# Kernel optimization log

Hardware: AMD Instinct MI355X
Metric: run time of the kernel (lower is better)

## Reference

```python
import jax, jax.numpy as jnp
import numpy as np

B, T_AUX, UP = 4, 75, 110
N_AUX, N_Q, HID, SKIP = 54, 256, 192, 256
K, AUX_K = 6, 3
DIL_FACTS = [0, 1, 2] * 3  # dilation_depth=3, dilation_repeat=3
T = T_AUX * UP - 1  # 8249


def conv1d(x, w, b, dil=1, pad=(0, 0)):
    # x: (B,C,T), w: (O,I,K) torch Conv1d layout
    if pad != (0, 0):
        x = jnp.pad(x, ((0, 0), (0, 0), pad))
    y = jax.lax.conv_general_dilated(x, w, (1,), 'VALID', rhs_dilation=(dil,),
                                     dimension_numbers=('NCH', 'OIH', 'NCH'))
    return y + b[None, :, None]


def setup_inputs() -> dict:
    key = jax.random.key(0)
    ks = jax.random.split(key, 24)
    s = 0.05
    inp = {
        'audio': jax.random.normal(ks[0], (B, N_Q, T), jnp.float32),
        'aux': jax.random.normal(ks[1], (B, N_AUX, T_AUX), jnp.float32),
        'scale_in_w': jax.random.normal(ks[2], (N_AUX, N_AUX, 1), jnp.float32) * s,
        'scale_in_b': jax.random.normal(ks[3], (N_AUX,), jnp.float32) * s,
        'aux0_w': jax.random.normal(ks[4], (N_AUX * 3, N_AUX, AUX_K), jnp.float32) * s,
        'aux0_b': jax.random.normal(ks[5], (N_AUX * 3,), jnp.float32) * s,
        'aux1_w': jax.random.normal(ks[6], (N_AUX * 9, N_AUX * 3, AUX_K), jnp.float32) * s,
        'aux1_b': jax.random.normal(ks[7], (N_AUX * 9,), jnp.float32) * s,
        'up_w': jax.random.normal(ks[8], (UP,), jnp.float32) * s,
        'up_b': jax.random.normal(ks[9], (), jnp.float32) * s,
        'causal_w': jax.random.normal(ks[10], (HID, N_Q, K), jnp.float32) * s,
        'causal_b': jax.random.normal(ks[11], (HID,), jnp.float32) * s,
        'inx_w': jax.random.normal(ks[12], (9, 2 * HID, N_AUX * 9, 1), jnp.float32) * s,
        'inx_b': jax.random.normal(ks[13], (9, 2 * HID), jnp.float32) * s,
        'dilh_w': jax.random.normal(ks[14], (9, 2 * HID, HID, K), jnp.float32) * s,
        'dilh_b': jax.random.normal(ks[15], (9, 2 * HID), jnp.float32) * s,
        'skip_w': jax.random.normal(ks[16], (9, SKIP, HID, 1), jnp.float32) * s,
        'skip_b': jax.random.normal(ks[17], (9, SKIP), jnp.float32) * s,
        'out1_w': jax.random.normal(ks[18], (N_Q, SKIP, 1), jnp.float32) * s,
        'out1_b': jax.random.normal(ks[19], (N_Q,), jnp.float32) * s,
        'out2_w': jax.random.normal(ks[20], (N_Q, N_Q, 1), jnp.float32) * s,
        'out2_b': jax.random.normal(ks[21], (N_Q,), jnp.float32) * s,
    }
    return inp


def reference(audio, aux, scale_in_w, scale_in_b, aux0_w, aux0_b, aux1_w, aux1_b,
              up_w, up_b, causal_w, causal_b, inx_w, inx_b, dilh_w, dilh_b,
              skip_w, skip_b, out1_w, out1_b, out2_w, out2_b):
    # conditioning path: scale_in -> two-sided dilated convs -> deconv upsample
    a = conv1d(aux, scale_in_w, scale_in_b)
    a = conv1d(a, aux0_w, aux0_b, dil=1, pad=(1, 1))      # k=3, dil=1, same length
    a = conv1d(a, aux1_w, aux1_b, dil=3, pad=(3, 3))      # k=3, dil=3, same length
    b_, c_, t_ = a.shape
    x = (a[:, :, :, None] * up_w).reshape(b_, c_, t_ * UP) + up_b  # ConvTranspose2d(1,1,(1,UP))
    x = x[:, :, 1:]  # (B, 486, T)
    # audio path: causal conv (left pad k-1) + softsign
    h = jax.nn.soft_sign(conv1d(audio, causal_w, causal_b, dil=1, pad=(K - 1, 0)))
    sum_out = None
    for l, d in enumerate(DIL_FACTS):
        dil = K ** d
        lpad = dil * (K - 1)  # k**(d+1) - k**d
        xh = conv1d(x, inx_w[l], inx_b[l]) * conv1d(h, dilh_w[l], dilh_b[l], dil=dil, pad=(lpad, 0))
        z = jax.nn.sigmoid(xh[:, :HID])
        h = (1.0 - z) * jnp.tanh(xh[:, HID:]) + z * h
        skip = conv1d(h, skip_w[l], skip_b[l])
        sum_out = skip if sum_out is None else sum_out + skip
    out = conv1d(jax.nn.relu(sum_out), out1_w, out1_b)
    out = conv1d(jax.nn.relu(out), out2_w, out2_b)
    return out.transpose(0, 2, 1)  # (B, T, n_quantize)
```

## Files before the change

kernel.cpp:

```cpp
#include <hip/hip_runtime.h>

#define TLEN 8249
#define TPAD 8320
#define NTILES 130
#define NB 4
#define NAUX 54
#define NQ 256
#define HID 192
#define NSKIP 256
#define KW 6
#define UPF 110
#define TAUX 75
#define PADR 180
#define HROWS (PADR + TPAD)

typedef __attribute__((ext_vector_type(8))) short bf16x8v;
typedef __attribute__((ext_vector_type(4))) float f32x4;

__device__ __forceinline__ unsigned short f2bf(float f) {
  unsigned int u = __float_as_uint(f);
  u += 0x7FFFu + ((u >> 16) & 1u);
  return (unsigned short)(u >> 16);
}

__device__ __forceinline__ f32x4 mfma16(bf16x8v a, bf16x8v b, f32x4 c) {
  return __builtin_amdgcn_mfma_f32_16x16x32_bf16(a, b, c, 0, 0, 0);
}

__global__ void prepack_kernel(
    const float* causal_w, const float* dilh_w, const float* skip_w,
    const float* out1_w, const float* out2_w,
    const float* inx_w, const float* inx_b, const float* up_b,
    unsigned short* pk_causal, unsigned short* pk_dilh, unsigned short* pk_skip,
    unsigned short* pk_out1, unsigned short* pk_out2, float* Cbuf)
{
  int i = blockIdx.x * blockDim.x + threadIdx.x;
  if (i < 9*6*6*24*64*8) {
    int t = i;
    int j = t & 7; t >>= 3;
    int lane = t & 63; t >>= 6;
    int nf = t % 24; t /= 24;
    int kc = t % 6; t /= 6;
    int tap = t % 6; t /= 6;
    int l = t;
    int oc = nf*16 + (lane & 15);
    int ic = kc*32 + ((lane >> 4) << 3) + j;
    pk_dilh[i] = f2bf(dilh_w[((l*384 + oc)*HID + ic)*KW + tap]);
  }
  if (i < 6*8*12*64*8) {
    int t = i;
    int j = t & 7; t >>= 3;
    int lane = t & 63; t >>= 6;
    int nf = t % 12; t /= 12;
    int kc = t % 8; t /= 8;
    int tap = t;
    int oc = nf*16 + (lane & 15);
    int ic = kc*32 + ((lane >> 4) << 3) + j;
    pk_causal[i] = f2bf(causal_w[(oc*NQ + ic)*KW + tap]);
  }
  if (i < 9*6*16*64*8) {
    int t = i;
    int j = t & 7; t >>= 3;
    int lane = t & 63; t >>= 6;
    int nf = t % 16; t /= 16;
    int kc = t % 6; t /= 6;
    int l = t;
    int sc = nf*16 + (lane & 15);
    int ic = kc*32 + ((lane >> 4) << 3) + j;
    pk_skip[i] = f2bf(skip_w[(l*NSKIP + sc)*HID + ic]);
  }
  if (i < 8*16*64*8) {
    int t = i;
    int j = t & 7; t >>= 3;
    int lane = t & 63; t >>= 6;
    int nf = t % 16; t /= 16;
    int kc = t;
    int oq = nf*16 + (lane & 15);
    int sc = kc*32 + ((lane >> 4) << 3) + j;
    pk_out1[i] = f2bf(out1_w[oq*NSKIP + sc]);
    pk_out2[i] = f2bf(out2_w[oq*NQ + sc]);
  }
  if (i < 9*384) {
    int l = i / 384, oc = i % 384;
    const float* wr = inx_w + (l*384 + oc)*486;
    float s = 0.f;
    for (int c = 0; c < 486; c++) s += wr[c];
    Cbuf[i] = up_b[0]*s + inx_b[i];
  }
}

__global__ void zpad_kernel(unsigned short* h_all) {
  int i = blockIdx.x*blockDim.x + threadIdx.x;
  if (i < 9*NB*PADR*HID) {
    int slab = i / (NB*PADR*HID), r = i % (NB*PADR*HID);
    int b = r / (PADR*HID), rr = r % (PADR*HID);
    h_all[((size_t)slab*NB + b)*HROWS*HID + rr] = 0;
  }
}

__global__ void aux1_kernel(const float* aux, const float* w, const float* bias, float* a1) {
  int q = blockIdx.x, b = blockIdx.y, co = threadIdx.x;
  if (co >= NAUX) return;
  float acc = bias[co];
  for (int ci = 0; ci < NAUX; ci++)
    acc += w[co*NAUX + ci] * aux[(b*NAUX + ci)*TAUX + q];
  a1[(b*NAUX + co)*TAUX + q] = acc;
}

__global__ void aux2_kernel(const float* a1, const float* w, const float* bias, float* a2) {
  __shared__ float s[3][NAUX];
  int q = blockIdx.x, b = blockIdx.y, tid = threadIdx.x;
  for (int i = tid; i < 3*NAUX; i += blockDim.x) {
    int k = i / NAUX, c = i % NAUX;
    int qq = q - 1 + k;
    s[k][c] = (qq >= 0 && qq < TAUX) ? a1[(b*NAUX + c)*TAUX + qq] : 0.f;
  }
  __syncthreads();
  int co = tid;
  if (co >= 162) return;
  float acc = bias[co];
  for (int c = 0; c < NAUX; c++)
    #pragma unroll
    for (int k = 0; k < 3; k++)
      acc += w[(co*NAUX + c)*3 + k] * s[k][c];
  a2[(b*162 + co)*TAUX + q] = acc;
}

__global__ void aux3_kernel(const float* a2, const float* w, const float* bias, float* a3) {
  __shared__ float s[3][162];
  int q = blockIdx.x, b = blockIdx.y, tid = threadIdx.x;
  for (int i = tid; i < 3*162; i += blockDim.x) {
    int k = i / 162, c = i % 162;
    int qq = q + 3*(k - 1);
    s[k][c] = (qq >= 0 && qq < TAUX) ? a2[(b*162 + c)*TAUX + qq] : 0.f;
  }
  __syncthreads();
  int co = tid;
  if (co >= 486) return;
  float acc = bias[co];
  for (int c = 0; c < 162; c++)
    #pragma unroll
    for (int k = 0; k < 3; k++)
      acc += w[(co*162 + c)*3 + k] * s[k][c];
  a3[(b*486 + co)*TAUX + q] = acc;
}

__global__ void g_kernel(const float* a3, const float* inx_w, float* G) {
  __shared__ float s[486][15];
  int q0 = blockIdx.x * 15, b = blockIdx.y, l = blockIdx.z;
  int tid = threadIdx.x;
  for (int i = tid; i < 486*15; i += 384) {
    int c = i / 15, qq = i % 15;
    s[c][qq] = a3[(b*486 + c)*TAUX + q0 + qq];
  }
  __syncthreads();
  int oc = tid;
  float acc[15];
  #pragma unroll
  for (int qq = 0; qq < 15; qq++) acc[qq] = 0.f;
  const float* wrow = inx_w + (l*384 + oc)*486;
  for (int c = 0; c < 486; c++) {
    float w = wrow[c];
    #pragma unroll
    for (int qq = 0; qq < 15; qq++) acc[qq] += w * s[c][qq];
  }
  for (int qq = 0; qq < 15; qq++)
    G[((size_t)(l*NB + b)*TAUX + q0 + qq)*384 + oc] = acc[qq];
}

__global__ __launch_bounds__(256, 2)
void causal_kernel(const float* audio, const unsigned short* pk, const float* cb,
                   unsigned short* hbf)
{
  __shared__ __align__(16) unsigned short sA[72*264];
  int b = blockIdx.y, t0 = blockIdx.x*64, tid = threadIdx.x;
  int wv = tid >> 6, lane = tid & 63, lanelo = lane & 15;

  for (int i = tid; i < 72*256; i += 256) {
    int ic = i / 72, tt = i % 72;
    int t = t0 - 5 + tt;
    float v = (t >= 0 && t < TLEN) ? audio[(size_t)(b*NQ + ic)*TLEN + t] : 0.f;
    sA[tt*264 + ic] = f2bf(v);
  }
  __syncthreads();

  f32x4 acc[4][3];
  f32x4 z4 = {0.f, 0.f, 0.f, 0.f};
  #pragma unroll
  for (int m = 0; m < 4; m++)
    #pragma unroll
    for (int i = 0; i < 3; i++) acc[m][i] = z4;

  for (int tap = 0; tap < 6; tap++) {
    for (int kc = 0; kc < 8; kc++) {
      bf16x8v A[4];
      int ko = kc*32 + ((lane >> 4) << 3);
      #pragma unroll
      for (int m = 0; m < 4; m++)
        A[m] = *(const bf16x8v*)&sA[(m*16 + lanelo + tap)*264 + ko];
      #pragma unroll
      for (int i = 0; i < 3; i++) {
        int nf = wv*3 + i;
        bf16x8v Bf = *(const bf16x8v*)&pk[(size_t)((((tap*8) + kc)*12 + nf)*64 + lane)*8];
        #pragma unroll
        for (int m = 0; m < 4; m++) acc[m][i] = mfma16(A[m], Bf, acc[m][i]);
      }
    }
  }

  #pragma unroll
  for (int m = 0; m < 4; m++)
    #pragma unroll
    for (int i = 0; i < 3; i++) {
      int oc = (wv*3 + i)*16 + lanelo;
      float bias = cb[oc];
      #pragma unroll
      for (int r = 0; r < 4; r++) {
        int tl = m*16 + ((lane >> 4) << 2) + r;
        int t = t0 + tl;
        float v = acc[m][i][r] + bias;
        float h0 = v / (1.f + fabsf(v));
        hbf[(size_t)(b*HROWS + t + PADR)*HID + oc] = f2bf(h0);
      }
    }
}

template<int DIL>
__device__ __forceinline__
void layer_u_body(const unsigned short* __restrict__ hin,
                  unsigned short* __restrict__ hout,
                  const unsigned short* __restrict__ pk_dilh_l,
                  const float* __restrict__ dilh_b_l,
                  const float* __restrict__ Gl, const float* __restrict__ Cl,
                  const float* __restrict__ up_w,
                  unsigned short* flat)
{
  int b = blockIdx.y, t0 = blockIdx.x*64, tid = threadIdx.x;
  int wv = tid >> 6, lane = tid & 63, lanelo = lane & 15, lanehi = lane >> 4;
  int mwv = wv >> 2, nwv = wv & 3;

  const size_t hbase = (size_t)b * HROWS * HID;
  int rowbase0 = t0 - 5*DIL + PADR;
  const int W = 64 + 5*DIL;

  for (int c = tid; c < W*24; c += 512) {
    int row = c/24, cbk = c%24;
    uint4 v = *(const uint4*)&hin[hbase + (size_t)(rowbase0+row)*HID + cbk*8];
    *(uint4*)&flat[row*192 + ((cbk ^ (row&7))<<3)] = v;
  }
  __syncthreads();

  f32x4 accz[2][3], acct[2][3];
  f32x4 z4 = {0.f, 0.f, 0.f, 0.f};
  #pragma unroll
  for (int m = 0; m < 2; m++)
    #pragma unroll
    for (int i = 0; i < 3; i++) { accz[m][i] = z4; acct[m][i] = z4; }

  for (int tap = 0; tap < 6; tap++) {
    #pragma unroll
    for (int kc = 0; kc < 6; kc++) {
      bf16x8v A[2];
      #pragma unroll
      for (int m = 0; m < 2; m++) {
        int r = mwv*32 + m*16 + lanelo + tap*DIL;
        int cbk = kc*4 + lanehi;
        A[m] = *(const bf16x8v*)&flat[r*192 + ((cbk ^ (r&7))<<3)];
      }
      #pragma unroll
      for (int i = 0; i < 3; i++) {
        const unsigned short* bp =
            &pk_dilh_l[(size_t)(((tap*6 + kc)*24 + nwv*3 + i)*64 + lane)*8];
        bf16x8v Bz = *(const bf16x8v*)bp;
        bf16x8v Bt = *(const bf16x8v*)(bp + 12*512);
        #pragma unroll
        for (int m = 0; m < 2; m++) {
          accz[m][i] = mfma16(A[m], Bz, accz[m][i]);
          acct[m][i] = mfma16(A[m], Bt, acct[m][i]);
        }
      }
    }
  }

  float izc[3], itc[3], bzc[3], btc[3];
  #pragma unroll
  for (int i = 0; i < 3; i++) {
    int ocz = (nwv*3 + i)*16 + lanelo;
    izc[i] = Cl[ocz];       itc[i] = Cl[192 + ocz];
    bzc[i] = dilh_b_l[ocz]; btc[i] = dilh_b_l[192 + ocz];
  }
  #pragma unroll
  for (int m = 0; m < 2; m++) {
    #pragma unroll
    for (int r = 0; r < 4; r++) {
      int tl = mwv*32 + m*16 + (lanehi << 2) + r;
      int t = t0 + tl;
      int hr = tl + 5*DIL;
      int tp1 = t + 1;
      int q = tp1 / UPF; if (q > TAUX - 1) q = TAUX - 1;
      int ui = tp1 - q*UPF; if (ui > UPF - 1) ui = UPF - 1;
      float u = up_w[ui];
      const float* Gb = Gl + (size_t)(b*TAUX + q)*384;
      #pragma unroll
      for (int i = 0; i < 3; i++) {
        int ocz = (nwv*3 + i)*16 + lanelo;
        float iz = u*Gb[ocz]       + izc[i];
        float it = u*Gb[192 + ocz] + itc[i];
        float xz = (accz[m][i][r] + bzc[i]) * iz;
        float xt = (acct[m][i][r] + btc[i]) * it;
        float z  = 1.f / (1.f + __expf(-xz));
        float e2 = __expf(2.f*xt);
        float th = 1.f - 2.f/(e2 + 1.f);
        int cbh = ocz >> 3, jh = ocz & 7;
        unsigned short hob = flat[hr*192 + ((cbh ^ (hr&7))<<3) + jh];
        float hold = __uint_as_float(((unsigned int)hob) << 16);
        float hn = (1.f - z)*th + z*hold;
        hout[hbase + (size_t)(t + PADR)*HID + ocz] = f2bf(hn);
      }
    }
  }
}

__global__ __launch_bounds__(512, 2)
void layer_u1_kernel(const unsigned short* __restrict__ hin,
                     unsigned short* __restrict__ hout,
                     const unsigned short* __restrict__ pk_dilh_l,
                     const float* __restrict__ dilh_b_l,
                     const float* __restrict__ Gl, const float* __restrict__ Cl,
                     const float* __restrict__ up_w)
{
  __shared__ __align__(16) unsigned short flat[69*192];
  layer_u_body<1>(hin, hout, pk_dilh_l, dilh_b_l, Gl, Cl, up_w, flat);
}

__global__ __launch_bounds__(512, 2)
void layer_u6_kernel(const unsigned short* __restrict__ hin,
                     unsigned short* __restrict__ hout,
                     const unsigned short* __restrict__ pk_dilh_l,
                     const float* __restrict__ dilh_b_l,
                     const float* __restrict__ Gl, const float* __restrict__ Cl,
                     const float* __restrict__ up_w)
{
  __shared__ __align__(16) unsigned short flat[94*192];
  layer_u_body<6>(hin, hout, pk_dilh_l, dilh_b_l, Gl, Cl, up_w, flat);
}

__global__ __launch_bounds__(512, 2)
void layer_d_kernel(const unsigned short* __restrict__ hin,
                    unsigned short* __restrict__ hout,
                    const unsigned short* __restrict__ pk_dilh_l,
                    const float* __restrict__ dilh_b_l,
                    const float* __restrict__ Gl, const float* __restrict__ Cl,
                    const float* __restrict__ up_w)
{
  __shared__ __align__(16) unsigned short hs[2][64*192];
  int b = blockIdx.y, t0 = blockIdx.x*64, tid = threadIdx.x;
  int wv = tid >> 6, lane = tid & 63, lanelo = lane & 15, lanehi = lane >> 4;
  int mwv = wv >> 2, nwv = wv & 3;

  const size_t hbase = (size_t)b * HROWS * HID;
  int rowbase0 = t0 - 180 + PADR;

  f32x4 accz[2][3], acct[2][3];
  f32x4 z4 = {0.f, 0.f, 0.f, 0.f};
  #pragma unroll
  for (int m = 0; m < 2; m++)
    #pragma unroll
    for (int i = 0; i < 3; i++) { accz[m][i] = z4; acct[m][i] = z4; }

  uint4 st[3];
  #pragma unroll
  for (int j = 0; j < 3; j++) {
    int c = tid + j*512, row = c/24, cbk = c%24;
    st[j] = *(const uint4*)&hin[hbase + (size_t)(rowbase0+row)*HID + cbk*8];
  }
  #pragma unroll
  for (int j = 0; j < 3; j++) {
    int c = tid + j*512, row = c/24, cbk = c%24;
    *(uint4*)&hs[0][row*192 + ((cbk ^ (row&7))<<3)] = st[j];
  }
  for (int tap = 0; tap < 6; tap++) {
    __syncthreads();
    if (tap < 5) {
      int rb = rowbase0 + (tap+1)*36;
      #pragma unroll
      for (int j = 0; j < 3; j++) {
        int c = tid + j*512, row = c/24, cbk = c%24;
        st[j] = *(const uint4*)&hin[hbase + (size_t)(rb+row)*HID + cbk*8];
      }
    }
    const unsigned short* bufc = hs[tap & 1];
    #pragma unroll
    for (int kc = 0; kc < 6; kc++) {
      bf16x8v A[2];
      #pragma unroll
      for (int m = 0; m < 2; m++) {
        int r = mwv*32 + m*16 + lanelo;
        int cbk = kc*4 + lanehi;
        A[m] = *(const bf16x8v*)&bufc[r*192 + ((cbk ^ (r&7))<<3)];
      }
      #pragma unroll
      for (int i = 0; i < 3; i++) {
        const unsigned short* bp =
            &pk_dilh_l[(size_t)(((tap*6 + kc)*24 + nwv*3 + i)*64 + lane)*8];
        bf16x8v Bz = *(const bf16x8v*)bp;
        bf16x8v Bt = *(const bf16x8v*)(bp + 12*512);
        #pragma unroll
        for (int m = 0; m < 2; m++) {
          accz[m][i] = mfma16(A[m], Bz, accz[m][i]);
          acct[m][i] = mfma16(A[m], Bt, acct[m][i]);
        }
      }
    }
    if (tap < 5) {
      unsigned short* bufn = hs[(tap+1) & 1];
      #pragma unroll
      for (int j = 0; j < 3; j++) {
        int c = tid + j*512, row = c/24, cbk = c%24;
        *(uint4*)&bufn[row*192 + ((cbk ^ (row&7))<<3)] = st[j];
      }
    }
  }

  float izc[3], itc[3], bzc[3], btc[3];
  #pragma unroll
  for (int i = 0; i < 3; i++) {
    int ocz = (nwv*3 + i)*16 + lanelo;
    izc[i] = Cl[ocz];       itc[i] = Cl[192 + ocz];
    bzc[i] = dilh_b_l[ocz]; btc[i] = dilh_b_l[192 + ocz];
  }
  #pragma unroll
  for (int m = 0; m < 2; m++) {
    #pragma unroll
    for (int r = 0; r < 4; r++) {
      int tl = mwv*32 + m*16 + (lanehi << 2) + r;
      int t = t0 + tl;
      int tp1 = t + 1;
      int q = tp1 / UPF; if (q > TAUX - 1) q = TAUX - 1;
      int ui = tp1 - q*UPF; if (ui > UPF - 1) ui = UPF - 1;
      float u = up_w[ui];
      const float* Gb = Gl + (size_t)(b*TAUX + q)*384;
      #pragma unroll
      for (int i = 0; i < 3; i++) {
        int ocz = (nwv*3 + i)*16 + lanelo;
        float iz = u*Gb[ocz]       + izc[i];
        float it = u*Gb[192 + ocz] + itc[i];
        float xz = (accz[m][i][r] + bzc[i]) * iz;
        float xt = (acct[m][i][r] + btc[i]) * it;
        float z  = 1.f / (1.f + __expf(-xz));
        float e2 = __expf(2.f*xt);
        float th = 1.f - 2.f/(e2 + 1.f);
        int cbh = ocz >> 3, jh = ocz & 7;
        unsigned short hob = hs[1][tl*192 + ((cbh ^ (tl&7))<<3) + jh];
        float hold = __uint_as_float(((unsigned int)hob) << 16);
        float hn = (1.f - z)*th + z*hold;
        hout[hbase + (size_t)(t + PADR)*HID + ocz] = f2bf(hn);
      }
    }
  }
}

__global__ __launch_bounds__(512, 2)
void tail_kernel(const unsigned short* __restrict__ h_all,
                 const unsigned short* __restrict__ pk_skip,
                 const float* __restrict__ skip_b,
                 const unsigned short* __restrict__ pk1, const float* __restrict__ b1,
                 const unsigned short* __restrict__ pk2, const float* __restrict__ b2,
                 float* __restrict__ dout)
{
  __shared__ __align__(16) unsigned short ss[2][64*192];
  int b = blockIdx.y, t0 = blockIdx.x*64, tid = threadIdx.x;
  int wv = tid >> 6, lane = tid & 63, lanelo = lane & 15, lanehi = lane >> 4;
  int mwv = wv >> 2, nwv = wv & 3;
  const size_t HS = (size_t)NB * HROWS * HID;
  f32x4 z4 = {0.f, 0.f, 0.f, 0.f};

  auto hsrc = [&](int l) {
    int slab = (l == 8) ? 0 : (l + 1);
    return h_all + (size_t)slab*HS + (size_t)b*HROWS*HID + (size_t)(t0 + PADR)*HID;
  };

  uint4 st[3];
  {
    const unsigned short* src = hsrc(0);
    #pragma unroll
    for (int j = 0; j < 3; j++) {
      int c = tid + j*512, row = c/24, cbk = c%24;
      st[j] = *(const uint4*)&src[(size_t)row*HID + cbk*8];
    }
    #pragma unroll
    for (int j = 0; j < 3; j++) {
      int c = tid + j*512, row = c/24, cbk = c%24;
      *(uint4*)&ss[0][row*192 + ((cbk ^ (row&7))<<3)] = st[j];
    }
  }

  f32x4 acc[2][4];
  #pragma unroll
  for (int m = 0; m < 2; m++)
    #pragma unroll
    for (int i = 0; i < 4; i++) acc[m][i] = z4;

  for (int l = 0; l < 9; l++) {
    __syncthreads();
    if (l < 8) {
      const unsigned short* src = hsrc(l + 1);
      #pragma unroll
      for (int j = 0; j < 3; j++) {
        int c = tid + j*512, row = c/24, cbk = c%24;
        st[j] = *(const uint4*)&src[(size_t)row*HID + cbk*8];
      }
    }
    const unsigned short* bufc = ss[l & 1];
    #pragma unroll
    for (int kc = 0; kc < 6; kc++) {
      bf16x8v A[2];
      #pragma unroll
      for (int m = 0; m < 2; m++) {
        int r = mwv*32 + m*16 + lanelo;
        int cbk = kc*4 + lanehi;
        A[m] = *(const bf16x8v*)&bufc[r*192 + ((cbk ^ (r&7))<<3)];
      }
      #pragma unroll
      for (int i = 0; i < 4; i++) {
        bf16x8v Bf = *(const bf16x8v*)
            &pk_skip[(size_t)(((l*6 + kc)*16 + nwv*4 + i)*64 + lane)*8];
        #pragma unroll
        for (int m = 0; m < 2; m++) acc[m][i] = mfma16(A[m], Bf, acc[m][i]);
      }
    }
    if (l < 8) {
      unsigned short* bufn = ss[(l+1) & 1];
      #pragma unroll
      for (int j = 0; j < 3; j++) {
        int c = tid + j*512, row = c/24, cbk = c%24;
        *(uint4*)&bufn[row*192 + ((cbk ^ (row&7))<<3)] = st[j];
      }
    }
  }
  __syncthreads();

  unsigned short* tile = &ss[0][0];
  #pragma unroll
  for (int i = 0; i < 4; i++) {
    int sc = (nwv*4 + i)*16 + lanelo;
    float bias = 0.f;
    #pragma unroll
    for (int l = 0; l < 9; l++) bias += skip_b[l*NSKIP + sc];
    #pragma unroll
    for (int m = 0; m < 2; m++) {
      #pragma unroll
      for (int r = 0; r < 4; r++) {
        int tl = mwv*32 + m*16 + (lanehi << 2) + r;
        tile[tl*264 + sc] = f2bf(fmaxf(acc[m][i][r] + bias, 0.f));
      }
    }
  }
  __syncthreads();

  #pragma unroll
  for (int m = 0; m < 2; m++)
    #pragma unroll
    for (int i = 0; i < 4; i++) acc[m][i] = z4;
  for (int kc = 0; kc < 8; kc++) {
    bf16x8v A[2];
    int ko = kc*32 + (lanehi << 3);
    #pragma unroll
    for (int m = 0; m < 2; m++)
      A[m] = *(const bf16x8v*)&tile[(mwv*32 + m*16 + lanelo)*264 + ko];
    #pragma unroll
    for (int i = 0; i < 4; i++) {
      bf16x8v Bf = *(const bf16x8v*)&pk1[(size_t)((kc*16 + nwv*4 + i)*64 + lane)*8];
      #pragma unroll
      for (int m = 0; m < 2; m++) acc[m][i] = mfma16(A[m], Bf, acc[m][i]);
    }
  }
  __syncthreads();
  #pragma unroll
  for (int m = 0; m < 2; m++)
    #pragma unroll
    for (int i = 0; i < 4; i++) {
      int oq = (nwv*4 + i)*16 + lanelo;
      float bias = b1[oq];
      #pragma unroll
      for (int r = 0; r < 4; r++) {
        int tl = mwv*32 + m*16 + (lanehi << 2) + r;
        tile[tl*264 + oq] = f2bf(fmaxf(acc[m][i][r] + bias, 0.f));
      }
    }
  __syncthreads();

  #pragma unroll
  for (int m = 0; m < 2; m++)
    #pragma unroll
    for (int i = 0; i < 4; i++) acc[m][i] = z4;
  for (int kc = 0; kc < 8; kc++) {
    bf16x8v A[2];
    int ko = kc*32 + (lanehi << 3);
    #pragma unroll
    for (int m = 0; m < 2; m++)
      A[m] = *(const bf16x8v*)&tile[(mwv*32 + m*16 + lanelo)*264 + ko];
    #pragma unroll
    for (int i = 0; i < 4; i++) {
      bf16x8v Bf = *(const bf16x8v*)&pk2[(size_t)((kc*16 + nwv*4 + i)*64 + lane)*8];
      #pragma unroll
      for (int m = 0; m < 2; m++) acc[m][i] = mfma16(A[m], Bf, acc[m][i]);
    }
  }
  float* so2 = (float*)&ss[0][0];
  #pragma unroll
  for (int p = 0; p < 2; p++) {
    __syncthreads();
    if (mwv == p) {
      #pragma unroll
      for (int m = 0; m < 2; m++) {
        #pragma unroll
        for (int i = 0; i < 4; i++) {
          int oq = (nwv*4 + i)*16 + lanelo;
          float bias = b2[oq];
          #pragma unroll
          for (int r = 0; r < 4; r++) {
            int lr = m*16 + (lanehi << 2) + r;
            so2[lr*260 + oq] = acc[m][i][r] + bias;
          }
        }
      }
    }
    __syncthreads();
    #pragma unroll
    for (int j = 0; j < 4; j++) {
      int c = tid + j*512, row = c >> 6, ch = c & 63;
      int t = t0 + p*32 + row;
      if (t < TLEN) {
        uint4 v = *(const uint4*)&so2[row*260 + ch*4];
        *(uint4*)&dout[(size_t)(b*TLEN + t)*NQ + ch*4] = v;
      }
    }
  }
}

extern "C" void kernel_launch(void* const* d_in, const int* in_sizes, int n_in,
                              void* d_out, int out_size, void* d_ws, size_t ws_size,
                              hipStream_t stream)
{
  const float* audio      = (const float*)d_in[0];
  const float* aux        = (const float*)d_in[1];
  const float* scale_in_w = (const float*)d_in[2];
  const float* scale_in_b = (const float*)d_in[3];
  const float* aux0_w     = (const float*)d_in[4];
  const float* aux0_b     = (const float*)d_in[5];
  const float* aux1_w     = (const float*)d_in[6];
  const float* aux1_b     = (const float*)d_in[7];
  const float* up_w       = (const float*)d_in[8];
  const float* up_b       = (const float*)d_in[9];
  const float* causal_w   = (const float*)d_in[10];
  const float* causal_b   = (const float*)d_in[11];
  const float* inx_w      = (const float*)d_in[12];
  const float* inx_b      = (const float*)d_in[13];
  const float* dilh_w     = (const float*)d_in[14];
  const float* dilh_b     = (const float*)d_in[15];
  const float* skip_w     = (const float*)d_in[16];
  const float* skip_b     = (const float*)d_in[17];
  const float* out1_w     = (const float*)d_in[18];
  const float* out1_b     = (const float*)d_in[19];
  const float* out2_w     = (const float*)d_in[20];
  const float* out2_b     = (const float*)d_in[21];

  char* ws = (char*)d_ws;
  size_t off = 0;
  auto alloc = [&](size_t bytes) -> void* {
    void* p = ws + off;
    off += (bytes + 255) & ~(size_t)255;
    return p;
  };
  unsigned short* pk_causal = (unsigned short*)alloc((size_t)6*8*12*64*8*2);
  unsigned short* pk_dilh   = (unsigned short*)alloc((size_t)9*6*6*24*64*8*2);
  unsigned short* pk_skip   = (unsigned short*)alloc((size_t)9*6*16*64*8*2);
  unsigned short* pk_out1   = (unsigned short*)alloc((size_t)8*16*64*8*2);
  unsigned short* pk_out2   = (unsigned short*)alloc((size_t)8*16*64*8*2);
  float* Cbuf    = (float*)alloc((size_t)9*384*4);
  float* a1      = (float*)alloc((size_t)NB*NAUX*TAUX*4);
  float* a2      = (float*)alloc((size_t)NB*162*TAUX*4);
  float* a3      = (float*)alloc((size_t)NB*486*TAUX*4);
  float* Gbuf    = (float*)alloc((size_t)9*NB*TAUX*384*4);
  const size_t HS = (size_t)NB*HROWS*HID;
  unsigned short* h_all = (unsigned short*)alloc((size_t)9*HS*2);

  hipLaunchKernelGGL(prepack_kernel, dim3((9*6*6*24*64*8 + 255)/256), dim3(256), 0, stream,
                     causal_w, dilh_w, skip_w, out1_w, out2_w, inx_w, inx_b, up_b,
                     pk_causal, pk_dilh, pk_skip, pk_out1, pk_out2, Cbuf);
  hipLaunchKernelGGL(zpad_kernel, dim3((9*NB*PADR*HID + 255)/256), dim3(256), 0, stream,
                     h_all);
  hipLaunchKernelGGL(aux1_kernel, dim3(TAUX, NB), dim3(64), 0, stream,
                     aux, scale_in_w, scale_in_b, a1);
  hipLaunchKernelGGL(aux2_kernel, dim3(TAUX, NB), dim3(192), 0, stream,
                     a1, aux0_w, aux0_b, a2);
  hipLaunchKernelGGL(aux3_kernel, dim3(TAUX, NB), dim3(512), 0, stream,
                     a2, aux1_w, aux1_b, a3);
  hipLaunchKernelGGL(g_kernel, dim3(5, NB, 9), dim3(384), 0, stream,
                     a3, inx_w, Gbuf);
  hipLaunchKernelGGL(causal_kernel, dim3(NTILES, NB), dim3(256), 0, stream,
                     audio, pk_causal, causal_b, h_all );

  const int dils[9] = {1, 6, 36, 1, 6, 36, 1, 6, 36};
  for (int l = 0; l < 9; l++) {
    const unsigned short* hin = h_all + (size_t)l*HS;
    unsigned short* hout      = (l == 8) ? h_all : h_all + (size_t)(l+1)*HS;
    const unsigned short* pkd = pk_dilh + (size_t)l*6*6*24*64*8;
    const float* dbl = dilh_b + (size_t)l*384;
    const float* Gl  = Gbuf + (size_t)l*NB*TAUX*384;
    const float* Cl  = Cbuf + (size_t)l*384;
    if (dils[l] == 1) {
      hipLaunchKernelGGL(layer_u1_kernel, dim3(NTILES, NB), dim3(512), 0, stream,
                         hin, hout, pkd, dbl, Gl, Cl, up_w);
    } else if (dils[l] == 6) {
      hipLaunchKernelGGL(layer_u6_kernel, dim3(NTILES, NB), dim3(512), 0, stream,
                         hin, hout, pkd, dbl, Gl, Cl, up_w);
    } else {
      hipLaunchKernelGGL(layer_d_kernel, dim3(NTILES, NB), dim3(512), 0, stream,
                         hin, hout, pkd, dbl, Gl, Cl, up_w);
    }
  }

  hipLaunchKernelGGL(tail_kernel, dim3(NTILES, NB), dim3(512), 0, stream,
                     h_all, pk_skip, skip_b, pk_out1, out1_b, pk_out2, out2_b,
                     (float*)d_out);
}
```

Baseline: 888.7 us.

## Process two batch elements per block to reuse weight fragments across batches

The layer and tail kernels now handle a pair of batch elements per block, so each packed weight fragment loaded from global memory feeds MFMAs for both batches. The grid shrinks from 4 to 2 in y, LDS is doubled through dynamic shared memory, and accumulator registers double. This aims to halve weight-fetch traffic per output. In exchange it halves the block count (260 blocks on a large GPU) and raises register pressure, which may hurt occupancy or cause spills under launch_bounds(512,2).

```diff
diff --git a/kernel.cpp b/kernel.cpp
--- a/kernel.cpp
+++ b/kernel.cpp
@@ -235,38 +235,43 @@
                   const float* __restrict__ up_w,
                   unsigned short* flat)
 {
-  int b = blockIdx.y, t0 = blockIdx.x*64, tid = threadIdx.x;
+  int pair = blockIdx.y, t0 = blockIdx.x*64, tid = threadIdx.x;
   int wv = tid >> 6, lane = tid & 63, lanelo = lane & 15, lanehi = lane >> 4;
   int mwv = wv >> 2, nwv = wv & 3;
 
-  const size_t hbase = (size_t)b * HROWS * HID;
+  const int W = 64 + 5*DIL;
   int rowbase0 = t0 - 5*DIL + PADR;
-  const int W = 64 + 5*DIL;
-
-  for (int c = tid; c < W*24; c += 512) {
-    int row = c/24, cbk = c%24;
-    uint4 v = *(const uint4*)&hin[hbase + (size_t)(rowbase0+row)*HID + cbk*8];
-    *(uint4*)&flat[row*192 + ((cbk ^ (row&7))<<3)] = v;
-  }
-  __syncthreads();
-
-  f32x4 accz[2][3], acct[2][3];
+
+  for (int c = tid; c < 2*W*24; c += 512) {
+    int bb = c / (W*24), rr = c % (W*24);
+    int row = rr/24, cbk = rr%24;
+    size_t hb = (size_t)(pair*2 + bb) * HROWS * HID;
+    uint4 v = *(const uint4*)&hin[hb + (size_t)(rowbase0+row)*HID + cbk*8];
+    *(uint4*)&flat[bb*(W*192) + row*192 + ((cbk ^ (row&7))<<3)] = v;
+  }
+  __syncthreads();
+
+  f32x4 accz[2][2][3], acct[2][2][3];
   f32x4 z4 = {0.f, 0.f, 0.f, 0.f};
   #pragma unroll
-  for (int m = 0; m < 2; m++)
-    #pragma unroll
-    for (int i = 0; i < 3; i++) { accz[m][i] = z4; acct[m][i] = z4; }
+  for (int bb = 0; bb < 2; bb++)
+    #pragma unroll
+    for (int m = 0; m < 2; m++)
+      #pragma unroll
+      for (int i = 0; i < 3; i++) { accz[bb][m][i] = z4; acct[bb][m][i] = z4; }
 
   for (int tap = 0; tap < 6; tap++) {
     #pragma unroll
     for (int kc = 0; kc < 6; kc++) {
-      bf16x8v A[2];
-      #pragma unroll
-      for (int m = 0; m < 2; m++) {
-        int r = mwv*32 + m*16 + lanelo + tap*DIL;
-        int cbk = kc*4 + lanehi;
-        A[m] = *(const bf16x8v*)&flat[r*192 + ((cbk ^ (r&7))<<3)];
-      }
+      bf16x8v A[2][2];
+      int cbk = kc*4 + lanehi;
+      #pragma unroll
+      for (int bb = 0; bb < 2; bb++)
+        #pragma unroll
+        for (int m = 0; m < 2; m++) {
+          int r = mwv*32 + m*16 + lanelo + tap*DIL;
+          A[bb][m] = *(const bf16x8v*)&flat[bb*(W*192) + r*192 + ((cbk ^ (r&7))<<3)];
+        }
       #pragma unroll
       for (int i = 0; i < 3; i++) {
         const unsigned short* bp =
@@ -274,10 +279,12 @@
         bf16x8v Bz = *(const bf16x8v*)bp;
         bf16x8v Bt = *(const bf16x8v*)(bp + 12*512);
         #pragma unroll
-        for (int m = 0; m < 2; m++) {
-          accz[m][i] = mfma16(A[m], Bz, accz[m][i]);
-          acct[m][i] = mfma16(A[m], Bt, acct[m][i]);
-        }
+        for (int bb = 0; bb < 2; bb++)
+          #pragma unroll
+          for (int m = 0; m < 2; m++) {
+            accz[bb][m][i] = mfma16(A[bb][m], Bz, accz[bb][m][i]);
+            acct[bb][m][i] = mfma16(A[bb][m], Bt, acct[bb][m][i]);
+          }
       }
     }
   }
@@ -290,32 +297,37 @@
     bzc[i] = dilh_b_l[ocz]; btc[i] = dilh_b_l[192 + ocz];
   }
   #pragma unroll
-  for (int m = 0; m < 2; m++) {
-    #pragma unroll
-    for (int r = 0; r < 4; r++) {
-      int tl = mwv*32 + m*16 + (lanehi << 2) + r;
-      int t = t0 + tl;
-      int hr = tl + 5*DIL;
-      int tp1 = t + 1;
-      int q = tp1 / UPF; if (q > TAUX - 1) q = TAUX - 1;
-      int ui = tp1 - q*UPF; if (ui > UPF - 1) ui = UPF - 1;
-      float u = up_w[ui];
-      const float* Gb = Gl + (size_t)(b*TAUX + q)*384;
-      #pragma unroll
-      for (int i = 0; i < 3; i++) {
-        int ocz = (nwv*3 + i)*16 + lanelo;
-        float iz = u*Gb[ocz]       + izc[i];
-        float it = u*Gb[192 + ocz] + itc[i];
-        float xz = (accz[m][i][r] + bzc[i]) * iz;
-        float xt = (acct[m][i][r] + btc[i]) * it;
-        float z  = 1.f / (1.f + __expf(-xz));
-        float e2 = __expf(2.f*xt);
-        float th = 1.f - 2.f/(e2 + 1.f);
-        int cbh = ocz >> 3, jh = ocz & 7;
-        unsigned short hob = flat[hr*192 + ((cbh ^ (hr&7))<<3) + jh];
-        float hold = __uint_as_float(((unsigned int)hob) << 16);
-        float hn = (1.f - z)*th + z*hold;
-        hout[hbase + (size_t)(t + PADR)*HID + ocz] = f2bf(hn);
+  for (int bb = 0; bb < 2; bb++) {
+    int b = pair*2 + bb;
+    size_t hb = (size_t)b * HROWS * HID;
+    #pragma unroll
+    for (int m = 0; m < 2; m++) {
+      #pragma unroll
+      for (int r = 0; r < 4; r++) {
+        int tl = mwv*32 + m*16 + (lanehi << 2) + r;
+        int t = t0 + tl;
+        int hr = tl + 5*DIL;
+        int tp1 = t + 1;
+        int q = tp1 / UPF; if (q > TAUX - 1) q = TAUX - 1;
+        int ui = tp1 - q*UPF; if (ui > UPF - 1) ui = UPF - 1;
+        float u = up_w[ui];
+        const float* Gb = Gl + (size_t)(b*TAUX + q)*384;
+        #pragma unroll
+        for (int i = 0; i < 3; i++) {
+          int ocz = (nwv*3 + i)*16 + lanelo;
+          float iz = u*Gb[ocz]       + izc[i];
+          float it = u*Gb[192 + ocz] + itc[i];
+          float xz = (accz[bb][m][i][r] + bzc[i]) * iz;
+          float xt = (acct[bb][m][i][r] + btc[i]) * it;
+          float z  = 1.f / (1.f + __expf(-xz));
+          float e2 = __expf(2.f*xt);
+          float th = 1.f - 2.f/(e2 + 1.f);
+          int cbh = ocz >> 3, jh = ocz & 7;
+          unsigned short hob = flat[bb*(W*192) + hr*192 + ((cbh ^ (hr&7))<<3) + jh];
+          float hold = __uint_as_float(((unsigned int)hob) << 16);
+          float hn = (1.f - z)*th + z*hold;
+          hout[hb + (size_t)(t + PADR)*HID + ocz] = f2bf(hn);
+        }
       }
     }
   }
@@ -329,8 +341,8 @@
                      const float* __restrict__ Gl, const float* __restrict__ Cl,
                      const float* __restrict__ up_w)
 {
-  __shared__ __align__(16) unsigned short flat[69*192];
-  layer_u_body<1>(hin, hout, pk_dilh_l, dilh_b_l, Gl, Cl, up_w, flat);
+  extern __shared__ __align__(16) unsigned short dynlds[];
+  layer_u_body<1>(hin, hout, pk_dilh_l, dilh_b_l, Gl, Cl, up_w, dynlds);
 }
 
 __global__ __launch_bounds__(512, 2)
@@ -341,8 +353,8 @@
                      const float* __restrict__ Gl, const float* __restrict__ Cl,
                      const float* __restrict__ up_w)
 {
-  __shared__ __align__(16) unsigned short flat[94*192];
-  layer_u_body<6>(hin, hout, pk_dilh_l, dilh_b_l, Gl, Cl, up_w, flat);
+  extern __shared__ __align__(16) unsigned short dynlds[];
+  layer_u_body<6>(hin, hout, pk_dilh_l, dilh_b_l, Gl, Cl, up_w, dynlds);
 }
 
 __global__ __launch_bounds__(512, 2)
@@ -353,52 +365,63 @@
                     const float* __restrict__ Gl, const float* __restrict__ Cl,
                     const float* __restrict__ up_w)
 {
-  __shared__ __align__(16) unsigned short hs[2][64*192];
-  int b = blockIdx.y, t0 = blockIdx.x*64, tid = threadIdx.x;
+  extern __shared__ __align__(16) unsigned short hs[];
+  int pair = blockIdx.y, t0 = blockIdx.x*64, tid = threadIdx.x;
   int wv = tid >> 6, lane = tid & 63, lanelo = lane & 15, lanehi = lane >> 4;
   int mwv = wv >> 2, nwv = wv & 3;
-
-  const size_t hbase = (size_t)b * HROWS * HID;
   int rowbase0 = t0 - 180 + PADR;
 
-  f32x4 accz[2][3], acct[2][3];
+  auto buf = [&](int bb, int p) { return hs + ((bb*2 + p)*64*192); };
+
+  f32x4 accz[2][2][3], acct[2][2][3];
   f32x4 z4 = {0.f, 0.f, 0.f, 0.f};
   #pragma unroll
-  for (int m = 0; m < 2; m++)
-    #pragma unroll
-    for (int i = 0; i < 3; i++) { accz[m][i] = z4; acct[m][i] = z4; }
-
-  uint4 st[3];
-  #pragma unroll
-  for (int j = 0; j < 3; j++) {
-    int c = tid + j*512, row = c/24, cbk = c%24;
-    st[j] = *(const uint4*)&hin[hbase + (size_t)(rowbase0+row)*HID + cbk*8];
-  }
-  #pragma unroll
-  for (int j = 0; j < 3; j++) {
-    int c = tid + j*512, row = c/24, cbk = c%24;
-    *(uint4*)&hs[0][row*192 + ((cbk ^ (row&7))<<3)] = st[j];
+  for (int bb = 0; bb < 2; bb++)
+    #pragma unroll
+    for (int m = 0; m < 2; m++)
+      #pragma unroll
+      for (int i = 0; i < 3; i++) { accz[bb][m][i] = z4; acct[bb][m][i] = z4; }
+
+  uint4 st[6];
+  #pragma unroll
+  for (int j = 0; j < 6; j++) {
+    int c = tid + j*512;
+    int bb = c / (64*24), rr = c % (64*24);
+    int row = rr/24, cbk = rr%24;
+    size_t hb = (size_t)(pair*2 + bb) * HROWS * HID;
+    st[j] = *(const uint4*)&hin[hb + (size_t)(rowbase0+row)*HID + cbk*8];
+  }
+  #pragma unroll
+  for (int j = 0; j < 6; j++) {
+    int c = tid + j*512;
+    int bb = c / (64*24), rr = c % (64*24);
+    int row = rr/24, cbk = rr%24;
+    *(uint4*)&buf(bb,0)[row*192 + ((cbk ^ (row&7))<<3)] = st[j];
   }
   for (int tap = 0; tap < 6; tap++) {
     __syncthreads();
     if (tap < 5) {
       int rb = rowbase0 + (tap+1)*36;
       #pragma unroll
-      for (int j = 0; j < 3; j++) {
-        int c = tid + j*512, row = c/24, cbk = c%24;
-        st[j] = *(const uint4*)&hin[hbase + (size_t)(rb+row)*HID + cbk*8];
-      }
-    }
-    const unsigned short* bufc = hs[tap & 1];
+      for (int j = 0; j < 6; j++) {
+        int c = tid + j*512;
+        int bb = c / (64*24), rr = c % (64*24);
+        int row = rr/24, cbk = rr%24;
+        size_t hb = (size_t)(pair*2 + bb) * HROWS * HID;
+        st[j] = *(const uint4*)&hin[hb + (size_t)(rb+row)*HID + cbk*8];
+      }
+    }
     #pragma unroll
     for (int kc = 0; kc < 6; kc++) {
-      bf16x8v A[2];
-      #pragma unroll
-      for (int m = 0; m < 2; m++) {
-        int r = mwv*32 + m*16 + lanelo;
-        int cbk = kc*4 + lanehi;
-        A[m] = *(const bf16x8v*)&bufc[r*192 + ((cbk ^ (r&7))<<3)];
-      }
+      bf16x8v A[2][2];
+      int cbk = kc*4 + lanehi;
+      #pragma unroll
+      for (int bb = 0; bb < 2; bb++)
+        #pragma unroll
+        for (int m = 0; m < 2; m++) {
+          int r = mwv*32 + m*16 + lanelo;
+          A[bb][m] = *(const bf16x8v*)&buf(bb, tap & 1)[r*192 + ((cbk ^ (r&7))<<3)];
+        }
       #pragma unroll
       for (int i = 0; i < 3; i++) {
         const unsigned short* bp =
@@ -406,18 +429,21 @@
         bf16x8v Bz = *(const bf16x8v*)bp;
         bf16x8v Bt = *(const bf16x8v*)(bp + 12*512);
         #pragma unroll
-        for (int m = 0; m < 2; m++) {
-          accz[m][i] = mfma16(A[m], Bz, accz[m][i]);
-          acct[m][i] = mfma16(A[m], Bt, acct[m][i]);
-        }
+        for (int bb = 0; bb < 2; bb++)
+          #pragma unroll
+          for (int m = 0; m < 2; m++) {
+            accz[bb][m][i] = mfma16(A[bb][m], Bz, accz[bb][m][i]);
+            acct[bb][m][i] = mfma16(A[bb][m], Bt, acct[bb][m][i]);
+          }
       }
     }
     if (tap < 5) {
-      unsigned short* bufn = hs[(tap+1) & 1];
-      #pragma unroll
-      for (int j = 0; j < 3; j++) {
-        int c = tid + j*512, row = c/24, cbk = c%24;
-        *(uint4*)&bufn[row*192 + ((cbk ^ (row&7))<<3)] = st[j];
+      #pragma unroll
+      for (int j = 0; j < 6; j++) {
+        int c = tid + j*512;
+        int bb = c / (64*24), rr = c % (64*24);
+        int row = rr/24, cbk = rr%24;
+        *(uint4*)&buf(bb, (tap+1) & 1)[row*192 + ((cbk ^ (row&7))<<3)] = st[j];
       }
     }
   }
@@ -430,31 +456,36 @@
     bzc[i] = dilh_b_l[ocz]; btc[i] = dilh_b_l[192 + ocz];
   }
   #pragma unroll
-  for (int m = 0; m < 2; m++) {
-    #pragma unroll
-    for (int r = 0; r < 4; r++) {
-      int tl = mwv*32 + m*16 + (lanehi << 2) + r;
-      int t = t0 + tl;
-      int tp1 = t + 1;
-      int q = tp1 / UPF; if (q > TAUX - 1) q = TAUX - 1;
-      int ui = tp1 - q*UPF; if (ui > UPF - 1) ui = UPF - 1;
-      float u = up_w[ui];
-      const float* Gb = Gl + (size_t)(b*TAUX + q)*384;
-      #pragma unroll
-      for (int i = 0; i < 3; i++) {
-        int ocz = (nwv*3 + i)*16 + lanelo;
-        float iz = u*Gb[ocz]       + izc[i];
-        float it = u*Gb[192 + ocz] + itc[i];
-        float xz = (accz[m][i][r] + bzc[i]) * iz;
-        float xt = (acct[m][i][r] + btc[i]) * it;
-        float z  = 1.f / (1.f + __expf(-xz));
-        float e2 = __expf(2.f*xt);
-        float th = 1.f - 2.f/(e2 + 1.f);
-        int cbh = ocz >> 3, jh = ocz & 7;
-        unsigned short hob = hs[1][tl*192 + ((cbh ^ (tl&7))<<3) + jh];
-        float hold = __uint_as_float(((unsigned int)hob) << 16);
-        float hn = (1.f - z)*th + z*hold;
-        hout[hbase + (size_t)(t + PADR)*HID + ocz] = f2bf(hn);
+  for (int bb = 0; bb < 2; bb++) {
+    int b = pair*2 + bb;
+    size_t hb = (size_t)b * HROWS * HID;
+    #pragma unroll
+    for (int m = 0; m < 2; m++) {
+      #pragma unroll
+      for (int r = 0; r < 4; r++) {
+        int tl = mwv*32 + m*16 + (lanehi << 2) + r;
+        int t = t0 + tl;
+        int tp1 = t + 1;
+        int q = tp1 / UPF; if (q > TAUX - 1) q = TAUX - 1;
+        int ui = tp1 - q*UPF; if (ui > UPF - 1) ui = UPF - 1;
+        float u = up_w[ui];
+        const float* Gb = Gl + (size_t)(b*TAUX + q)*384;
+        #pragma unroll
+        for (int i = 0; i < 3; i++) {
+          int ocz = (nwv*3 + i)*16 + lanelo;
+          float iz = u*Gb[ocz]       + izc[i];
+          float it = u*Gb[192 + ocz] + itc[i];
+          float xz = (accz[bb][m][i][r] + bzc[i]) * iz;
+          float xt = (acct[bb][m][i][r] + btc[i]) * it;
+          float z  = 1.f / (1.f + __expf(-xz));
+          float e2 = __expf(2.f*xt);
+          float th = 1.f - 2.f/(e2 + 1.f);
+          int cbh = ocz >> 3, jh = ocz & 7;
+          unsigned short hob = buf(bb,1)[tl*192 + ((cbh ^ (tl&7))<<3) + jh];
+          float hold = __uint_as_float(((unsigned int)hob) << 16);
+          float hn = (1.f - z)*th + z*hold;
+          hout[hb + (size_t)(t + PADR)*HID + ocz] = f2bf(hn);
+        }
       }
     }
   }
@@ -468,79 +499,89 @@
                  const unsigned short* __restrict__ pk2, const float* __restrict__ b2,
                  float* __restrict__ dout)
 {
-  __shared__ __align__(16) unsigned short ss[2][64*192];
-  int b = blockIdx.y, t0 = blockIdx.x*64, tid = threadIdx.x;
+  extern __shared__ __align__(16) unsigned short ss[];
+  int pair = blockIdx.y, t0 = blockIdx.x*64, tid = threadIdx.x;
   int wv = tid >> 6, lane = tid & 63, lanelo = lane & 15, lanehi = lane >> 4;
   int mwv = wv >> 2, nwv = wv & 3;
   const size_t HS = (size_t)NB * HROWS * HID;
   f32x4 z4 = {0.f, 0.f, 0.f, 0.f};
 
-  auto hsrc = [&](int l) {
+  auto buf = [&](int bb, int p) { return ss + ((bb*2 + p)*64*192); };
+  auto hsrc = [&](int l, int bb) {
     int slab = (l == 8) ? 0 : (l + 1);
-    return h_all + (size_t)slab*HS + (size_t)b*HROWS*HID + (size_t)(t0 + PADR)*HID;
+    return h_all + (size_t)slab*HS + (size_t)(pair*2+bb)*HROWS*HID
+                 + (size_t)(t0 + PADR)*HID;
   };
 
-  uint4 st[3];
-  {
-    const unsigned short* src = hsrc(0);
-    #pragma unroll
-    for (int j = 0; j < 3; j++) {
-      int c = tid + j*512, row = c/24, cbk = c%24;
-      st[j] = *(const uint4*)&src[(size_t)row*HID + cbk*8];
-    }
-    #pragma unroll
-    for (int j = 0; j < 3; j++) {
-      int c = tid + j*512, row = c/24, cbk = c%24;
-      *(uint4*)&ss[0][row*192 + ((cbk ^ (row&7))<<3)] = st[j];
-    }
-  }
-
-  f32x4 acc[2][4];
-  #pragma unroll
-  for (int m = 0; m < 2; m++)
-    #pragma unroll
-    for (int i = 0; i < 4; i++) acc[m][i] = z4;
+  uint4 st[6];
+  #pragma unroll
+  for (int j = 0; j < 6; j++) {
+    int c = tid + j*512;
+    int bb = c / (64*24), rr = c % (64*24);
+    int row = rr/24, cbk = rr%24;
+    st[j] = *(const uint4*)&hsrc(0,bb)[(size_t)row*HID + cbk*8];
+  }
+  #pragma unroll
+  for (int j = 0; j < 6; j++) {
+    int c = tid + j*512;
+    int bb = c / (64*24), rr = c % (64*24);
+    int row = rr/24, cbk = rr%24;
+    *(uint4*)&buf(bb,0)[row*192 + ((cbk ^ (row&7))<<3)] = st[j];
+  }
+
+  f32x4 acc[2][2][4];
+  #pragma unroll
+  for (int bb = 0; bb < 2; bb++)
+    #pragma unroll
+    for (int m = 0; m < 2; m++)
+      #pragma unroll
+      for (int i = 0; i < 4; i++) acc[bb][m][i] = z4;
 
   for (int l = 0; l < 9; l++) {
     __syncthreads();
     if (l < 8) {
-      const unsigned short* src = hsrc(l + 1);
-      #pragma unroll
-      for (int j = 0; j < 3; j++) {
-        int c = tid + j*512, row = c/24, cbk = c%24;
-        st[j] = *(const uint4*)&src[(size_t)row*HID + cbk*8];
-      }
-    }
-    const unsigned short* bufc = ss[l & 1];
+      #pragma unroll
+      for (int j = 0; j < 6; j++) {
+        int c = tid + j*512;
+        int bb = c / (64*24), rr = c % (64*24);
+        int row = rr/24, cbk = rr%24;
+        st[j] = *(const uint4*)&hsrc(l+1,bb)[(size_t)row*HID + cbk*8];
+      }
+    }
     #pragma unroll
     for (int kc = 0; kc < 6; kc++) {
-      bf16x8v A[2];
-      #pragma unroll
-      for (int m = 0; m < 2; m++) {
-        int r = mwv*32 + m*16 + lanelo;
-        int cbk = kc*4 + lanehi;
-        A[m] = *(const bf16x8v*)&bufc[r*192 + ((cbk ^ (r&7))<<3)];
-      }
+      bf16x8v A[2][2];
+      int cbk = kc*4 + lanehi;
+      #pragma unroll
+      for (int bb = 0; bb < 2; bb++)
+        #pragma unroll
+        for (int m = 0; m < 2; m++) {
+          int r = mwv*32 + m*16 + lanelo;
+          A[bb][m] = *(const bf16x8v*)&buf(bb, l & 1)[r*192 + ((cbk ^ (r&7))<<3)];
+        }
       #pragma unroll
       for (int i = 0; i < 4; i++) {
         bf16x8v Bf = *(const bf16x8v*)
             &pk_skip[(size_t)(((l*6 + kc)*16 + nwv*4 + i)*64 + lane)*8];
         #pragma unroll
-        for (int m = 0; m < 2; m++) acc[m][i] = mfma16(A[m], Bf, acc[m][i]);
+        for (int bb = 0; bb < 2; bb++)
+          #pragma unroll
+          for (int m = 0; m < 2; m++) acc[bb][m][i] = mfma16(A[bb][m], Bf, acc[bb][m][i]);
       }
     }
     if (l < 8) {
-      unsigned short* bufn = ss[(l+1) & 1];
-      #pragma unroll
-      for (int j = 0; j < 3; j++) {
-        int c = tid + j*512, row = c/24, cbk = c%24;
-        *(uint4*)&bufn[row*192 + ((cbk ^ (row&7))<<3)] = st[j];
-      }
-    }
-  }
-  __syncthreads();
-
-  unsigned short* tile = &ss[0][0];
+      #pragma unroll
+      for (int j = 0; j < 6; j++) {
+        int c = tid + j*512;
+        int bb = c / (64*24), rr = c % (64*24);
+        int row = rr/24, cbk = rr%24;
+        *(uint4*)&buf(bb, (l+1) & 1)[row*192 + ((cbk ^ (row&7))<<3)] = st[j];
+      }
+    }
+  }
+  __syncthreads();
+
+  auto tile = [&](int bb) { return ss + bb*(64*264); };
   #pragma unroll
   for (int i = 0; i < 4; i++) {
     int sc = (nwv*4 + i)*16 + lanelo;
@@ -548,92 +589,111 @@
     #pragma unroll
     for (int l = 0; l < 9; l++) bias += skip_b[l*NSKIP + sc];
     #pragma unroll
-    for (int m = 0; m < 2; m++) {
-      #pragma unroll
-      for (int r = 0; r < 4; r++) {
-        int tl = mwv*32 + m*16 + (lanehi << 2) + r;
-        tile[tl*264 + sc] = f2bf(fmaxf(acc[m][i][r] + bias, 0.f));
-      }
-    }
-  }
-  __syncthreads();
-
-  #pragma unroll
-  for (int m = 0; m < 2; m++)
-    #pragma unroll
-    for (int i = 0; i < 4; i++) acc[m][i] = z4;
+    for (int bb = 0; bb < 2; bb++)
+      #pragma unroll
+      for (int m = 0; m < 2; m++) {
+        #pragma unroll
+        for (int r = 0; r < 4; r++) {
+          int tl = mwv*32 + m*16 + (lanehi << 2) + r;
+          tile(bb)[tl*264 + sc] = f2bf(fmaxf(acc[bb][m][i][r] + bias, 0.f));
+        }
+      }
+  }
+  __syncthreads();
+
+  #pragma unroll
+  for (int bb = 0; bb < 2; bb++)
+    #pragma unroll
+    for (int m = 0; m < 2; m++)
+      #pragma unroll
+      for (int i = 0; i < 4; i++) acc[bb][m][i] = z4;
   for (int kc = 0; kc < 8; kc++) {
-    bf16x8v A[2];
+    bf16x8v A[2][2];
     int ko = kc*32 + (lanehi << 3);
     #pragma unroll
-    for (int m = 0; m < 2; m++)
-      A[m] = *(const bf16x8v*)&tile[(mwv*32 + m*16 + lanelo)*264 + ko];
+    for (int bb = 0; bb < 2; bb++)
+      #pragma unroll
+      for (int m = 0; m < 2; m++)
+        A[bb][m] = *(const bf16x8v*)&tile(bb)[(mwv*32 + m*16 + lanelo)*264 + ko];
     #pragma unroll
     for (int i = 0; i < 4; i++) {
       bf16x8v Bf = *(const bf16x8v*)&pk1[(size_t)((kc*16 + nwv*4 + i)*64 + lane)*8];
       #pragma unroll
-      for (int m = 0; m < 2; m++) acc[m][i] = mfma16(A[m], Bf, acc[m][i]);
-    }
-  }
-  __syncthreads();
-  #pragma unroll
-  for (int m = 0; m < 2; m++)
-    #pragma unroll
-    for (int i = 0; i < 4; i++) {
-      int oq = (nwv*4 + i)*16 + lanelo;
-      float bias = b1[oq];
-      #pragma unroll
-      for (int r = 0; r < 4; r++) {
-        int tl = mwv*32 + m*16 + (lanehi << 2) + r;
-        tile[tl*264 + oq] = f2bf(fmaxf(acc[m][i][r] + bias, 0.f));
-      }
-    }
-  __syncthreads();
-
-  #pragma unroll
-  for (int m = 0; m < 2; m++)
-    #pragma unroll
-    for (int i = 0; i < 4; i++) acc[m][i] = z4;
+      for (int bb = 0; bb < 2; bb++)
+        #pragma unroll
+        for (int m = 0; m < 2; m++) acc[bb][m][i] = mfma16(A[bb][m], Bf, acc[bb][m][i]);
+    }
+  }
+  __syncthreads();
+  #pragma unroll
+  for (int bb = 0; bb < 2; bb++)
+    #pragma unroll
+    for (int m = 0; m < 2; m++)
+      #pragma unroll
+      for (int i = 0; i < 4; i++) {
+        int oq = (nwv*4 + i)*16 + lanelo;
+        float bias = b1[oq];
+        #pragma unroll
+        for (int r = 0; r < 4; r++) {
+          int tl = mwv*32 + m*16 + (lanehi << 2) + r;
+          tile(bb)[tl*264 + oq] = f2bf(fmaxf(acc[bb][m][i][r] + bias, 0.f));
+        }
+      }
+  __syncthreads();
+
+  #pragma unroll
+  for (int bb = 0; bb < 2; bb++)
+    #pragma unroll
+    for (int m = 0; m < 2; m++)
+      #pragma unroll
+      for (int i = 0; i < 4; i++) acc[bb][m][i] = z4;
   for (int kc = 0; kc < 8; kc++) {
-    bf16x8v A[2];
+    bf16x8v A[2][2];
     int ko = kc*32 + (lanehi << 3);
     #pragma unroll
-    for (int m = 0; m < 2; m++)
-      A[m] = *(const bf16x8v*)&tile[(mwv*32 + m*16 + lanelo)*264 + ko];
+    for (int bb = 0; bb < 2; bb++)
+      #pragma unroll
+      for (int m = 0; m < 2; m++)
+        A[bb][m] = *(const bf16x8v*)&tile(bb)[(mwv*32 + m*16 + lanelo)*264 + ko];
     #pragma unroll
     for (int i = 0; i < 4; i++) {
       bf16x8v Bf = *(const bf16x8v*)&pk2[(size_t)((kc*16 + nwv*4 + i)*64 + lane)*8];
       #pragma unroll
-      for (int m = 0; m < 2; m++) acc[m][i] = mfma16(A[m], Bf, acc[m][i]);
-    }
-  }
-  float* so2 = (float*)&ss[0][0];
+      for (int bb = 0; bb < 2; bb++)
+        #pragma unroll
+        for (int m = 0; m < 2; m++) acc[bb][m][i] = mfma16(A[bb][m], Bf, acc[bb][m][i]);
+    }
+  }
+  float* so2 = (float*)ss;
   #pragma unroll
   for (int p = 0; p < 2; p++) {
     __syncthreads();
     if (mwv == p) {
       #pragma unroll
-      for (int m = 0; m < 2; m++) {
-        #pragma unroll
-        for (int i = 0; i < 4; i++) {
-          int oq = (nwv*4 + i)*16 + lanelo;
-          float bias = b2[oq];
+      for (int bb = 0; bb < 2; bb++)
+        #pragma unroll
+        for (int m = 0; m < 2; m++)
           #pragma unroll
-          for (int r = 0; r < 4; r++) {
-            int lr = m*16 + (lanehi << 2) + r;
-            so2[lr*260 + oq] = acc[m][i][r] + bias;
+          for (int i = 0; i < 4; i++) {
+            int oq = (nwv*4 + i)*16 + lanelo;
+            float bias = b2[oq];
+            #pragma unroll
+            for (int r = 0; r < 4; r++) {
+              int lr = m*16 + (lanehi << 2) + r;
+              so2[bb*(32*260) + lr*260 + oq] = acc[bb][m][i][r] + bias;
+            }
           }
-        }
-      }
     }
     __syncthreads();
     #pragma unroll
-    for (int j = 0; j < 4; j++) {
-      int c = tid + j*512, row = c >> 6, ch = c & 63;
+    for (int j = 0; j < 8; j++) {
+      int c = tid + j*512;
+      int bb = c >> 11, rr = c & 2047;
+      int row = rr >> 6, ch = rr & 63;
       int t = t0 + p*32 + row;
       if (t < TLEN) {
-        uint4 v = *(const uint4*)&so2[row*260 + ch*4];
-        *(uint4*)&dout[(size_t)(b*TLEN + t)*NQ + ch*4] = v;
+        uint4 v = *(const uint4*)&so2[bb*(32*260) + row*260 + ch*4];
+        *(uint4*)&dout[(size_t)((pair*2+bb)*TLEN + t)*NQ + ch*4] = v;
       }
     }
   }
@@ -686,6 +746,15 @@
   const size_t HS = (size_t)NB*HROWS*HID;
   unsigned short* h_all = (unsigned short*)alloc((size_t)9*HS*2);
 
+  hipFuncSetAttribute((const void*)layer_u1_kernel,
+                      hipFuncAttributeMaxDynamicSharedMemorySize, 2*69*192*2);
+  hipFuncSetAttribute((const void*)layer_u6_kernel,
+                      hipFuncAttributeMaxDynamicSharedMemorySize, 2*94*192*2);
+  hipFuncSetAttribute((const void*)layer_d_kernel,
+                      hipFuncAttributeMaxDynamicSharedMemorySize, 4*64*192*2);
+  hipFuncSetAttribute((const void*)tail_kernel,
+                      hipFuncAttributeMaxDynamicSharedMemorySize, 4*64*192*2);
+
   hipLaunchKernelGGL(prepack_kernel, dim3((9*6*6*24*64*8 + 255)/256), dim3(256), 0, stream,
                      causal_w, dilh_w, skip_w, out1_w, out2_w, inx_w, inx_b, up_b,
                      pk_causal, pk_dilh, pk_skip, pk_out1, pk_out2, Cbuf);
@@ -711,18 +780,18 @@
     const float* Gl  = Gbuf + (size_t)l*NB*TAUX*384;
     const float* Cl  = Cbuf + (size_t)l*384;
     if (dils[l] == 1) {
-      hipLaunchKernelGGL(layer_u1_kernel, dim3(NTILES, NB), dim3(512), 0, stream,
-                         hin, hout, pkd, dbl, Gl, Cl, up_w);
+      hipLaunchKernelGGL(layer_u1_kernel, dim3(NTILES, 2), dim3(512),
+                         2*69*192*2, stream, hin, hout, pkd, dbl, Gl, Cl, up_w);
     } else if (dils[l] == 6) {
-      hipLaunchKernelGGL(layer_u6_kernel, dim3(NTILES, NB), dim3(512), 0, stream,
-                         hin, hout, pkd, dbl, Gl, Cl, up_w);
+      hipLaunchKernelGGL(layer_u6_kernel, dim3(NTILES, 2), dim3(512),
+                         2*94*192*2, stream, hin, hout, pkd, dbl, Gl, Cl, up_w);
     } else {
-      hipLaunchKernelGGL(layer_d_kernel, dim3(NTILES, NB), dim3(512), 0, stream,
-                         hin, hout, pkd, dbl, Gl, Cl, up_w);
-    }
-  }
-
-  hipLaunchKernelGGL(tail_kernel, dim3(NTILES, NB), dim3(512), 0, stream,
+      hipLaunchKernelGGL(layer_d_kernel, dim3(NTILES, 2), dim3(512),
+                         4*64*192*2, stream, hin, hout, pkd, dbl, Gl, Cl, up_w);
+    }
+  }
+
+  hipLaunchKernelGGL(tail_kernel, dim3(NTILES, 2), dim3(512), 4*64*192*2, stream,
                      h_all, pk_skip, skip_b, pk_out1, out1_b, pk_out2, out2_b,
                      (float*)d_out);
 }
```

After: 1.137 ms. 27.9% more time.
